# Performance work log

Hardware: AMD Instinct MI355X
Metric: run time of the kernel (lower is better)

Reference implementation:

```python
import jax, jax.numpy as jnp
import numpy as np

D = 64          # d_in
NH = [256, 256] # nn_depth_design
L = 16          # flow_layers
B = 32768       # batch of samples


def _build_masks():
    # Deterministic mask maps: this_min=0, this_max=d_in-1 for all layers
    mh0 = np.arange(NH[0]) % (D - 1)
    mh1 = np.arange(NH[1]) % (D - 1)
    M1 = (mh0[None, :] <= mh1[:, None]).astype(np.float32)  # [nh1, nh0]
    M0s, M2s = [], []
    for l in range(L):
        perm = np.arange(D) if l % 2 == 0 else np.arange(D)[::-1]
        M0s.append((perm[None, :] <= mh0[:, None]).astype(np.float32))  # [nh0, D]
        M2s.append((mh1[None, :] < perm[:, None]).astype(np.float32))  # [D, nh1]
    M0 = np.stack(M0s)                                   # [L, nh0, D]
    M1 = np.broadcast_to(M1, (L,) + M1.shape).copy()     # [L, nh1, nh0]
    M2 = np.stack(M2s)                                   # [L, D, nh1]
    return jnp.asarray(M0), jnp.asarray(M1), jnp.asarray(M2)


def setup_inputs() -> dict:
    key = jax.random.key(0)
    ks = jax.random.split(key, 13)
    u = jax.random.normal(ks[0], (B, D), dtype=jnp.float32)

    def w(k, shape, fan_in):
        return jax.random.uniform(k, shape, jnp.float32, -1.0, 1.0) / np.sqrt(fan_in)

    inp = {"u": u}
    i = 1
    for net in ("loc", "scale"):
        inp[f"{net}_W0"] = w(ks[i], (L, NH[0], D), D); i += 1
        inp[f"{net}_b0"] = w(ks[i], (L, NH[0]), D); i += 1
        inp[f"{net}_W1"] = w(ks[i], (L, NH[1], NH[0]), NH[0]); i += 1
        inp[f"{net}_b1"] = w(ks[i], (L, NH[1]), NH[0]); i += 1
        inp[f"{net}_W2"] = w(ks[i], (L, D, NH[1]), NH[1]); i += 1
        inp[f"{net}_b2"] = w(ks[i], (L, D), NH[1]); i += 1
    M0, M1, M2 = _build_masks()
    inp["M0"], inp["M1"], inp["M2"] = M0, M1, M2
    return inp


def reference(u, loc_W0, loc_b0, loc_W1, loc_b1, loc_W2, loc_b2,
              scale_W0, scale_b0, scale_W1, scale_b1, scale_W2, scale_b2,
              M0, M1, M2):
    def step(y, p):
        (lW0, lb0, lW1, lb1, lW2, lb2,
         sW0, sb0, sW1, sb1, sW2, sb2, m0, m1, m2) = p

        def net(W0, b0, W1, b1, W2, b2):
            h = jax.nn.relu(y @ (m0 * W0).T + b0)    # [B, nh0]
            h = jax.nn.relu(h @ (m1 * W1).T + b1)    # [B, nh1]
            return h @ (m2 * W2).T + b2              # [B, D]

        loc = net(lW0, lb0, lW1, lb1, lW2, lb2)
        sc = net(sW0, sb0, sW1, sb1, sW2, sb2)
        # inverse=False coupling: exp(-scale) * (y - loc)
        return jnp.exp(-sc) * (y - loc), None

    params = (loc_W0, loc_b0, loc_W1, loc_b1, loc_W2, loc_b2,
              scale_W0, scale_b0, scale_W1, scale_b1, scale_W2, scale_b2,
              M0, M1, M2)
    y, _ = jax.lax.scan(step, u, params)
    return y
```

## Files before the change

### kernel.cpp

```cpp
#include <hip/hip_runtime.h>
#include <hip/hip_bf16.h>

typedef __bf16 bf16x8 __attribute__((ext_vector_type(8)));
typedef __bf16 bf16x4 __attribute__((ext_vector_type(4)));
typedef float  f32x4  __attribute__((ext_vector_type(4)));

#define LAYERS 16
#define DIM 64
#define NHID 256
#define BATCH 32768
#define MTILE 64
#define NBLOCKS (BATCH / MTILE)

#define W0P_PER 16384
#define W1P_PER 65536
#define W2P_PER 16384
#define W0P_TOT (32 * W0P_PER)
#define W1P_TOT (32 * W1P_PER)
#define W2P_TOT (32 * W2P_PER)
#define PACK_TOT (W0P_TOT + W1P_TOT + W2P_TOT)

__global__ __launch_bounds__(256) void pack_weights(
    const float* __restrict__ lW0, const float* __restrict__ lW1, const float* __restrict__ lW2,
    const float* __restrict__ sW0, const float* __restrict__ sW1, const float* __restrict__ sW2,
    const float* __restrict__ M0,  const float* __restrict__ M1,  const float* __restrict__ M2,
    __bf16* __restrict__ ws)
{
    const long i = ((long)blockIdx.x * 256 + threadIdx.x) * 8;
    const float* W; const float* M; long src;
    if (i < W0P_TOT) {
        int netl = (int)(i / W0P_PER), rem = (int)(i % W0P_PER);
        int net = netl >> 4, l = netl & 15;
        int nt = rem >> 10, kt = (rem >> 9) & 1, lane = (rem >> 3) & 63;
        int n = nt * 16 + (lane & 15), k = kt * 32 + (lane >> 4) * 8;
        W = net ? sW0 : lW0; M = M0;
        src = (long)(l * 256 + n) * 64 + k;
    } else if (i < W0P_TOT + W1P_TOT) {
        long r = i - W0P_TOT;
        int netl = (int)(r / W1P_PER), rem = (int)(r % W1P_PER);
        int net = netl >> 4, l = netl & 15;
        int nt = rem >> 12, kt = (rem >> 9) & 7, lane = (rem >> 3) & 63;
        int n = nt * 16 + (lane & 15), k = kt * 32 + (lane >> 4) * 8;
        W = net ? sW1 : lW1; M = M1;
        src = (long)(l * 256 + n) * 256 + k;
    } else {
        long r = i - W0P_TOT - W1P_TOT;
        int netl = (int)(r / W2P_PER), rem = (int)(r % W2P_PER);
        int net = netl >> 4, l = netl & 15;
        int nt = rem >> 12, kt = (rem >> 9) & 7, lane = (rem >> 3) & 63;
        int n = nt * 16 + (lane & 15), k = kt * 32 + (lane >> 4) * 8;
        W = net ? sW2 : lW2; M = M2;
        src = (long)(l * 64 + n) * 256 + k;
    }
    f32x4 wa = *(const f32x4*)(W + src);
    f32x4 wb = *(const f32x4*)(W + src + 4);
    f32x4 ma = *(const f32x4*)(M + src);
    f32x4 mb = *(const f32x4*)(M + src + 4);
    bf16x8 o;
    o[0] = (__bf16)(wa[0] * ma[0]); o[1] = (__bf16)(wa[1] * ma[1]);
    o[2] = (__bf16)(wa[2] * ma[2]); o[3] = (__bf16)(wa[3] * ma[3]);
    o[4] = (__bf16)(wb[0] * mb[0]); o[5] = (__bf16)(wb[1] * mb[1]);
    o[6] = (__bf16)(wb[2] * mb[2]); o[7] = (__bf16)(wb[3] * mb[3]);
    *(bf16x8*)(ws + i) = o;
}

__global__ __launch_bounds__(512, 4) void flow_kernel(
    const float* __restrict__ u,
    const __bf16* __restrict__ wp,
    const float* __restrict__ lb0, const float* __restrict__ lb1, const float* __restrict__ lb2,
    const float* __restrict__ sb0, const float* __restrict__ sb1, const float* __restrict__ sb2,
    float* __restrict__ out)
{
    __shared__ __bf16 ybf[MTILE][72];
    __shared__ __bf16 buf1[MTILE][264];
    __shared__ __bf16 buf2[MTILE][264];

    const int tid  = threadIdx.x;
    const int wave = tid >> 6;
    const int lane = tid & 63;
    const int quad = lane >> 4;
    const int l16  = lane & 15;
    const int blk  = blockIdx.x;

    const int whid = wave * 2;
    const int mt3  = wave >> 1;
    const int ntb  = (wave & 1) * 2;

    const __bf16* w0p = wp;
    const __bf16* w1p = wp + W0P_TOT;
    const __bf16* w2p = wp + W0P_TOT + W1P_TOT;

    float y[2][4];
    #pragma unroll
    for (int ntl = 0; ntl < 2; ++ntl) {
        const float* src = u + (long)(blk * MTILE + (ntb + ntl) * 16 + l16) * DIM
                             + mt3 * 16 + quad * 4;
        f32x4 t = *(const f32x4*)src;
        #pragma unroll
        for (int r = 0; r < 4; ++r) y[ntl][r] = t[r];
    }

    for (int l = 0; l < LAYERS; ++l) {
        #pragma unroll
        for (int ntl = 0; ntl < 2; ++ntl) {
            bf16x4 v;
            #pragma unroll
            for (int r = 0; r < 4; ++r) v[r] = (__bf16)y[ntl][r];
            *(bf16x4*)&ybf[(ntb + ntl) * 16 + l16][mt3 * 16 + quad * 4] = v;
        }
        __syncthreads();

        float locr[2][4], scr[2][4];

        #pragma unroll
        for (int net = 0; net < 2; ++net) {
            const __bf16* w0b = w0p + (long)(net * 16 + l) * W0P_PER;
            const __bf16* w1b = w1p + (long)(net * 16 + l) * W1P_PER;
            const __bf16* w2b = w2p + (long)(net * 16 + l) * W2P_PER;
            const float* b0 = (net ? sb0 : lb0) + l * 256;
            const float* b1 = (net ? sb1 : lb1) + l * 256;
            const float* b2 = (net ? sb2 : lb2) + l * 64;

            {
                f32x4 acc[2][4];
                #pragma unroll
                for (int mt = 0; mt < 2; ++mt)
                    #pragma unroll
                    for (int nt = 0; nt < 4; ++nt)
                        acc[mt][nt] = (f32x4){0.f, 0.f, 0.f, 0.f};
                #pragma unroll
                for (int kt = 0; kt < 2; ++kt) {
                    bf16x8 aw[2], bv[4];
                    #pragma unroll
                    for (int mt = 0; mt < 2; ++mt)
                        aw[mt] = *(const bf16x8*)(w0b + (long)((whid + mt) * 2 + kt) * 512 + lane * 8);
                    #pragma unroll
                    for (int nt = 0; nt < 4; ++nt)
                        bv[nt] = *(const bf16x8*)&ybf[nt * 16 + l16][kt * 32 + quad * 8];
                    #pragma unroll
                    for (int mt = 0; mt < 2; ++mt)
                        #pragma unroll
                        for (int nt = 0; nt < 4; ++nt)
                            acc[mt][nt] = __builtin_amdgcn_mfma_f32_16x16x32_bf16(aw[mt], bv[nt], acc[mt][nt], 0, 0, 0);
                }
                #pragma unroll
                for (int mt = 0; mt < 2; ++mt) {
                    f32x4 bias = *(const f32x4*)(b0 + (whid + mt) * 16 + quad * 4);
                    #pragma unroll
                    for (int nt = 0; nt < 4; ++nt) {
                        bf16x4 v;
                        #pragma unroll
                        for (int r = 0; r < 4; ++r)
                            v[r] = (__bf16)fmaxf(acc[mt][nt][r] + bias[r], 0.f);
                        *(bf16x4*)&buf1[nt * 16 + l16][(whid + mt) * 16 + quad * 4] = v;
                    }
                }
            }
            __syncthreads();

            {
                f32x4 acc[2][4];
                #pragma unroll
                for (int mt = 0; mt < 2; ++mt)
                    #pragma unroll
                    for (int nt = 0; nt < 4; ++nt)
                        acc[mt][nt] = (f32x4){0.f, 0.f, 0.f, 0.f};
                #pragma unroll
                for (int kt = 0; kt < 8; ++kt) {
                    bf16x8 aw[2], bv[4];
                    #pragma unroll
                    for (int mt = 0; mt < 2; ++mt)
                        aw[mt] = *(const bf16x8*)(w1b + (long)((whid + mt) * 8 + kt) * 512 + lane * 8);
                    #pragma unroll
                    for (int nt = 0; nt < 4; ++nt)
                        bv[nt] = *(const bf16x8*)&buf1[nt * 16 + l16][kt * 32 + quad * 8];
                    #pragma unroll
                    for (int mt = 0; mt < 2; ++mt)
                        #pragma unroll
                        for (int nt = 0; nt < 4; ++nt)
                            acc[mt][nt] = __builtin_amdgcn_mfma_f32_16x16x32_bf16(aw[mt], bv[nt], acc[mt][nt], 0, 0, 0);
                }
                #pragma unroll
                for (int mt = 0; mt < 2; ++mt) {
                    f32x4 bias = *(const f32x4*)(b1 + (whid + mt) * 16 + quad * 4);
                    #pragma unroll
                    for (int nt = 0; nt < 4; ++nt) {
                        bf16x4 v;
                        #pragma unroll
                        for (int r = 0; r < 4; ++r)
                            v[r] = (__bf16)fmaxf(acc[mt][nt][r] + bias[r], 0.f);
                        *(bf16x4*)&buf2[nt * 16 + l16][(whid + mt) * 16 + quad * 4] = v;
                    }
                }
            }
            __syncthreads();

            {
                f32x4 acc[2];
                acc[0] = (f32x4){0.f, 0.f, 0.f, 0.f};
                acc[1] = (f32x4){0.f, 0.f, 0.f, 0.f};
                #pragma unroll
                for (int kt = 0; kt < 8; ++kt) {
                    bf16x8 aw = *(const bf16x8*)(w2b + (long)(mt3 * 8 + kt) * 512 + lane * 8);
                    #pragma unroll
                    for (int ntl = 0; ntl < 2; ++ntl) {
                        bf16x8 bv = *(const bf16x8*)&buf2[(ntb + ntl) * 16 + l16][kt * 32 + quad * 8];
                        acc[ntl] = __builtin_amdgcn_mfma_f32_16x16x32_bf16(aw, bv, acc[ntl], 0, 0, 0);
                    }
                }
                f32x4 bias = *(const f32x4*)(b2 + mt3 * 16 + quad * 4);
                if (net == 0) {
                    #pragma unroll
                    for (int ntl = 0; ntl < 2; ++ntl)
                        #pragma unroll
                        for (int r = 0; r < 4; ++r)
                            locr[ntl][r] = acc[ntl][r] + bias[r];
                } else {
                    #pragma unroll
                    for (int ntl = 0; ntl < 2; ++ntl)
                        #pragma unroll
                        for (int r = 0; r < 4; ++r)
                            scr[ntl][r] = acc[ntl][r] + bias[r];
                }
            }
        }

        #pragma unroll
        for (int ntl = 0; ntl < 2; ++ntl)
            #pragma unroll
            for (int r = 0; r < 4; ++r)
                y[ntl][r] = __expf(-scr[ntl][r]) * (y[ntl][r] - locr[ntl][r]);
    }

    #pragma unroll
    for (int ntl = 0; ntl < 2; ++ntl) {
        f32x4 t;
        #pragma unroll
        for (int r = 0; r < 4; ++r) t[r] = y[ntl][r];
        float* dst = out + (long)(blk * MTILE + (ntb + ntl) * 16 + l16) * DIM
                         + mt3 * 16 + quad * 4;
        *(f32x4*)dst = t;
    }
}

extern "C" void kernel_launch(void* const* d_in, const int* in_sizes, int n_in,
                              void* d_out, int out_size, void* d_ws, size_t ws_size,
                              hipStream_t stream) {
    const float* u   = (const float*)d_in[0];
    const float* lW0 = (const float*)d_in[1];
    const float* lb0 = (const float*)d_in[2];
    const float* lW1 = (const float*)d_in[3];
    const float* lb1 = (const float*)d_in[4];
    const float* lW2 = (const float*)d_in[5];
    const float* lb2 = (const float*)d_in[6];
    const float* sW0 = (const float*)d_in[7];
    const float* sb0 = (const float*)d_in[8];
    const float* sW1 = (const float*)d_in[9];
    const float* sb1 = (const float*)d_in[10];
    const float* sW2 = (const float*)d_in[11];
    const float* sb2 = (const float*)d_in[12];
    const float* M0  = (const float*)d_in[13];
    const float* M1  = (const float*)d_in[14];
    const float* M2  = (const float*)d_in[15];

    if (ws_size < (size_t)PACK_TOT * sizeof(__bf16)) return;
    __bf16* ws = (__bf16*)d_ws;

    pack_weights<<<PACK_TOT / 8 / 256, 256, 0, stream>>>(
        lW0, lW1, lW2, sW0, sW1, sW2, M0, M1, M2, ws);
    flow_kernel<<<NBLOCKS, 512, 0, stream>>>(
        u, ws, lb0, lb1, lb2, sb0, sb1, sb2, (float*)d_out);
}
```

Before: 369.7 us.

## Prefetch next-stage weight fragments into registers ahead of the barrier

Global weight fragments are now loaded one GEMM stage early. The first half of W1 is fetched during the W0 epilogue, W2 and the next W0 during the W1 epilogue, and the first W0 before the layer loop. This hides global and L2 load latency behind MFMA work and the __syncthreads barriers instead of stalling at the start of each GEMM. The cost is higher register pressure (about 20 extra bf16x8 values held), which could lower occupancy or cause spills. The next-W0 index wraps to layer 16 on the final iteration, which looks like an out-of-range read, though the result is never used.

```diff
diff --git a/kernel.cpp b/kernel.cpp
--- a/kernel.cpp
+++ b/kernel.cpp
@@ -19,6 +19,8 @@
 #define W1P_TOT (32 * W1P_PER)
 #define W2P_TOT (32 * W2P_PER)
 #define PACK_TOT (W0P_TOT + W1P_TOT + W2P_TOT)
+
+__device__ __forceinline__ bf16x8 ldw(const __bf16* p) { return *(const bf16x8*)p; }
 
 __global__ __launch_bounds__(256) void pack_weights(
     const float* __restrict__ lW0, const float* __restrict__ lW1, const float* __restrict__ lW2,
@@ -100,6 +102,13 @@
         for (int r = 0; r < 4; ++r) y[ntl][r] = t[r];
     }
 
+    bf16x8 wg1[4];
+    #pragma unroll
+    for (int mt = 0; mt < 2; ++mt)
+        #pragma unroll
+        for (int kt = 0; kt < 2; ++kt)
+            wg1[mt * 2 + kt] = ldw(w0p + (long)((whid + mt) * 2 + kt) * 512 + lane * 8);
+
     for (int l = 0; l < LAYERS; ++l) {
         #pragma unroll
         for (int ntl = 0; ntl < 2; ++ntl) {
@@ -114,13 +123,15 @@
 
         #pragma unroll
         for (int net = 0; net < 2; ++net) {
-            const __bf16* w0b = w0p + (long)(net * 16 + l) * W0P_PER;
             const __bf16* w1b = w1p + (long)(net * 16 + l) * W1P_PER;
             const __bf16* w2b = w2p + (long)(net * 16 + l) * W2P_PER;
+            const __bf16* w0n = w0p + (long)(net == 0 ? 16 + l : l + 1) * W0P_PER;
             const float* b0 = (net ? sb0 : lb0) + l * 256;
             const float* b1 = (net ? sb1 : lb1) + l * 256;
             const float* b2 = (net ? sb2 : lb2) + l * 64;
 
+            bf16x8 wg2a[8];
+
             {
                 f32x4 acc[2][4];
                 #pragma unroll
@@ -130,10 +141,7 @@
                         acc[mt][nt] = (f32x4){0.f, 0.f, 0.f, 0.f};
                 #pragma unroll
                 for (int kt = 0; kt < 2; ++kt) {
-                    bf16x8 aw[2], bv[4];
-                    #pragma unroll
-                    for (int mt = 0; mt < 2; ++mt)
-                        aw[mt] = *(const bf16x8*)(w0b + (long)((whid + mt) * 2 + kt) * 512 + lane * 8);
+                    bf16x8 bv[4];
                     #pragma unroll
                     for (int nt = 0; nt < 4; ++nt)
                         bv[nt] = *(const bf16x8*)&ybf[nt * 16 + l16][kt * 32 + quad * 8];
@@ -141,8 +149,13 @@
                     for (int mt = 0; mt < 2; ++mt)
                         #pragma unroll
                         for (int nt = 0; nt < 4; ++nt)
-                            acc[mt][nt] = __builtin_amdgcn_mfma_f32_16x16x32_bf16(aw[mt], bv[nt], acc[mt][nt], 0, 0, 0);
-                }
+                            acc[mt][nt] = __builtin_amdgcn_mfma_f32_16x16x32_bf16(wg1[mt * 2 + kt], bv[nt], acc[mt][nt], 0, 0, 0);
+                }
+                #pragma unroll
+                for (int kt = 0; kt < 4; ++kt)
+                    #pragma unroll
+                    for (int mt = 0; mt < 2; ++mt)
+                        wg2a[kt * 2 + mt] = ldw(w1b + (long)((whid + mt) * 8 + kt) * 512 + lane * 8);
                 #pragma unroll
                 for (int mt = 0; mt < 2; ++mt) {
                     f32x4 bias = *(const f32x4*)(b0 + (whid + mt) * 16 + quad * 4);
@@ -158,6 +171,8 @@
             }
             __syncthreads();
 
+            bf16x8 wg3[8];
+
             {
                 f32x4 acc[2][4];
                 #pragma unroll
@@ -167,10 +182,12 @@
                         acc[mt][nt] = (f32x4){0.f, 0.f, 0.f, 0.f};
                 #pragma unroll
                 for (int kt = 0; kt < 8; ++kt) {
-                    bf16x8 aw[2], bv[4];
-                    #pragma unroll
-                    for (int mt = 0; mt < 2; ++mt)
-                        aw[mt] = *(const bf16x8*)(w1b + (long)((whid + mt) * 8 + kt) * 512 + lane * 8);
+                    bf16x8 aw[2];
+                    #pragma unroll
+                    for (int mt = 0; mt < 2; ++mt)
+                        aw[mt] = (kt < 4) ? wg2a[kt * 2 + mt]
+                                          : ldw(w1b + (long)((whid + mt) * 8 + kt) * 512 + lane * 8);
+                    bf16x8 bv[4];
                     #pragma unroll
                     for (int nt = 0; nt < 4; ++nt)
                         bv[nt] = *(const bf16x8*)&buf1[nt * 16 + l16][kt * 32 + quad * 8];
@@ -180,6 +197,14 @@
                         for (int nt = 0; nt < 4; ++nt)
                             acc[mt][nt] = __builtin_amdgcn_mfma_f32_16x16x32_bf16(aw[mt], bv[nt], acc[mt][nt], 0, 0, 0);
                 }
+                #pragma unroll
+                for (int kt = 0; kt < 8; ++kt)
+                    wg3[kt] = ldw(w2b + (long)(mt3 * 8 + kt) * 512 + lane * 8);
+                #pragma unroll
+                for (int mt = 0; mt < 2; ++mt)
+                    #pragma unroll
+                    for (int kt = 0; kt < 2; ++kt)
+                        wg1[mt * 2 + kt] = ldw(w0n + (long)((whid + mt) * 2 + kt) * 512 + lane * 8);
                 #pragma unroll
                 for (int mt = 0; mt < 2; ++mt) {
                     f32x4 bias = *(const f32x4*)(b1 + (whid + mt) * 16 + quad * 4);
@@ -201,11 +226,10 @@
                 acc[1] = (f32x4){0.f, 0.f, 0.f, 0.f};
                 #pragma unroll
                 for (int kt = 0; kt < 8; ++kt) {
-                    bf16x8 aw = *(const bf16x8*)(w2b + (long)(mt3 * 8 + kt) * 512 + lane * 8);
                     #pragma unroll
                     for (int ntl = 0; ntl < 2; ++ntl) {
                         bf16x8 bv = *(const bf16x8*)&buf2[(ntb + ntl) * 16 + l16][kt * 32 + quad * 8];
-                        acc[ntl] = __builtin_amdgcn_mfma_f32_16x16x32_bf16(aw, bv, acc[ntl], 0, 0, 0);
+                        acc[ntl] = __builtin_amdgcn_mfma_f32_16x16x32_bf16(wg3[kt], bv, acc[ntl], 0, 0, 0);
                     }
                 }
                 f32x4 bias = *(const f32x4*)(b2 + mt3 * 16 + quad * 4);
```

Result: faster. 349.9 us (-5.4%).

## Double waves per block and halve per-wave MFMA tile

Applied to the files above, without the earlier changes.

Launches 1024-thread blocks so 16 waves split each 64-row tile: each wave computes a 2x2 grid of 16x16 tiles in the hidden layers and one 16x16 tile in the output layer. This raises parallelism and latency hiding per block and reduces per-wave register pressure. In exchange, each weight fragment is now loaded by two waves (one per batch half), so global/L2 weight traffic and barrier cost grow.

```diff
diff --git a/kernel.cpp b/kernel.cpp
--- a/kernel.cpp
+++ b/kernel.cpp
@@ -19,6 +19,8 @@
 #define W1P_TOT (32 * W1P_PER)
 #define W2P_TOT (32 * W2P_PER)
 #define PACK_TOT (W0P_TOT + W1P_TOT + W2P_TOT)
+
+__device__ __forceinline__ bf16x8 ldw(const __bf16* p) { return *(const bf16x8*)p; }
 
 __global__ __launch_bounds__(256) void pack_weights(
     const float* __restrict__ lW0, const float* __restrict__ lW1, const float* __restrict__ lW2,
@@ -64,7 +66,7 @@
     *(bf16x8*)(ws + i) = o;
 }
 
-__global__ __launch_bounds__(512, 4) void flow_kernel(
+__global__ __launch_bounds__(1024, 8) void flow_kernel(
     const float* __restrict__ u,
     const __bf16* __restrict__ wp,
     const float* __restrict__ lb0, const float* __restrict__ lb1, const float* __restrict__ lb2,
@@ -82,35 +84,28 @@
     const int l16  = lane & 15;
     const int blk  = blockIdx.x;
 
-    const int whid = wave * 2;
-    const int mt3  = wave >> 1;
-    const int ntb  = (wave & 1) * 2;
+    const int g   = wave >> 1;
+    const int p   = wave & 1;
+    const int ot3 = wave >> 2;
+    const int bt3 = wave & 3;
 
     const __bf16* w0p = wp;
     const __bf16* w1p = wp + W0P_TOT;
     const __bf16* w2p = wp + W0P_TOT + W1P_TOT;
 
-    float y[2][4];
-    #pragma unroll
-    for (int ntl = 0; ntl < 2; ++ntl) {
-        const float* src = u + (long)(blk * MTILE + (ntb + ntl) * 16 + l16) * DIM
-                             + mt3 * 16 + quad * 4;
-        f32x4 t = *(const f32x4*)src;
-        #pragma unroll
-        for (int r = 0; r < 4; ++r) y[ntl][r] = t[r];
-    }
+    f32x4 y = *(const f32x4*)(u + (long)(blk * MTILE + bt3 * 16 + l16) * DIM
+                                + ot3 * 16 + quad * 4);
 
     for (int l = 0; l < LAYERS; ++l) {
-        #pragma unroll
-        for (int ntl = 0; ntl < 2; ++ntl) {
+        {
             bf16x4 v;
             #pragma unroll
-            for (int r = 0; r < 4; ++r) v[r] = (__bf16)y[ntl][r];
-            *(bf16x4*)&ybf[(ntb + ntl) * 16 + l16][mt3 * 16 + quad * 4] = v;
+            for (int r = 0; r < 4; ++r) v[r] = (__bf16)y[r];
+            *(bf16x4*)&ybf[bt3 * 16 + l16][ot3 * 16 + quad * 4] = v;
         }
         __syncthreads();
 
-        float locr[2][4], scr[2][4];
+        f32x4 locr, scr;
 
         #pragma unroll
         for (int net = 0; net < 2; ++net) {
@@ -122,125 +117,105 @@
             const float* b2 = (net ? sb2 : lb2) + l * 64;
 
             {
-                f32x4 acc[2][4];
-                #pragma unroll
-                for (int mt = 0; mt < 2; ++mt)
-                    #pragma unroll
-                    for (int nt = 0; nt < 4; ++nt)
-                        acc[mt][nt] = (f32x4){0.f, 0.f, 0.f, 0.f};
+                f32x4 acc[2][2];
+                #pragma unroll
+                for (int o = 0; o < 2; ++o)
+                    #pragma unroll
+                    for (int b = 0; b < 2; ++b)
+                        acc[o][b] = (f32x4){0.f, 0.f, 0.f, 0.f};
                 #pragma unroll
                 for (int kt = 0; kt < 2; ++kt) {
-                    bf16x8 aw[2], bv[4];
-                    #pragma unroll
-                    for (int mt = 0; mt < 2; ++mt)
-                        aw[mt] = *(const bf16x8*)(w0b + (long)((whid + mt) * 2 + kt) * 512 + lane * 8);
-                    #pragma unroll
-                    for (int nt = 0; nt < 4; ++nt)
-                        bv[nt] = *(const bf16x8*)&ybf[nt * 16 + l16][kt * 32 + quad * 8];
-                    #pragma unroll
-                    for (int mt = 0; mt < 2; ++mt)
-                        #pragma unroll
-                        for (int nt = 0; nt < 4; ++nt)
-                            acc[mt][nt] = __builtin_amdgcn_mfma_f32_16x16x32_bf16(aw[mt], bv[nt], acc[mt][nt], 0, 0, 0);
-                }
-                #pragma unroll
-                for (int mt = 0; mt < 2; ++mt) {
-                    f32x4 bias = *(const f32x4*)(b0 + (whid + mt) * 16 + quad * 4);
-                    #pragma unroll
-                    for (int nt = 0; nt < 4; ++nt) {
+                    bf16x8 aw[2], bv[2];
+                    #pragma unroll
+                    for (int o = 0; o < 2; ++o)
+                        aw[o] = ldw(w0b + (long)((2 * g + o) * 2 + kt) * 512 + lane * 8);
+                    #pragma unroll
+                    for (int b = 0; b < 2; ++b)
+                        bv[b] = *(const bf16x8*)&ybf[(2 * p + b) * 16 + l16][kt * 32 + quad * 8];
+                    #pragma unroll
+                    for (int o = 0; o < 2; ++o)
+                        #pragma unroll
+                        for (int b = 0; b < 2; ++b)
+                            acc[o][b] = __builtin_amdgcn_mfma_f32_16x16x32_bf16(aw[o], bv[b], acc[o][b], 0, 0, 0);
+                }
+                #pragma unroll
+                for (int o = 0; o < 2; ++o) {
+                    f32x4 bias = *(const f32x4*)(b0 + (2 * g + o) * 16 + quad * 4);
+                    #pragma unroll
+                    for (int b = 0; b < 2; ++b) {
                         bf16x4 v;
                         #pragma unroll
                         for (int r = 0; r < 4; ++r)
-                            v[r] = (__bf16)fmaxf(acc[mt][nt][r] + bias[r], 0.f);
-                        *(bf16x4*)&buf1[nt * 16 + l16][(whid + mt) * 16 + quad * 4] = v;
+                            v[r] = (__bf16)fmaxf(acc[o][b][r] + bias[r], 0.f);
+                        *(bf16x4*)&buf1[(2 * p + b) * 16 + l16][(2 * g + o) * 16 + quad * 4] = v;
                     }
                 }
             }
             __syncthreads();
 
             {
-                f32x4 acc[2][4];
-                #pragma unroll
-                for (int mt = 0; mt < 2; ++mt)
-                    #pragma unroll
-                    for (int nt = 0; nt < 4; ++nt)
-                        acc[mt][nt] = (f32x4){0.f, 0.f, 0.f, 0.f};
+                f32x4 acc[2][2];
+                #pragma unroll
+                for (int o = 0; o < 2; ++o)
+                    #pragma unroll
+                    for (int b = 0; b < 2; ++b)
+                        acc[o][b] = (f32x4){0.f, 0.f, 0.f, 0.f};
                 #pragma unroll
                 for (int kt = 0; kt < 8; ++kt) {
-                    bf16x8 aw[2], bv[4];
-                    #pragma unroll
-                    for (int mt = 0; mt < 2; ++mt)
-                        aw[mt] = *(const bf16x8*)(w1b + (long)((whid + mt) * 8 + kt) * 512 + lane * 8);
-                    #pragma unroll
-                    for (int nt = 0; nt < 4; ++nt)
-                        bv[nt] = *(const bf16x8*)&buf1[nt * 16 + l16][kt * 32 + quad * 8];
-                    #pragma unroll
-                    for (int mt = 0; mt < 2; ++mt)
-                        #pragma unroll
-                        for (int nt = 0; nt < 4; ++nt)
-                            acc[mt][nt] = __builtin_amdgcn_mfma_f32_16x16x32_bf16(aw[mt], bv[nt], acc[mt][nt], 0, 0, 0);
-                }
-                #pragma unroll
-                for (int mt = 0; mt < 2; ++mt) {
-                    f32x4 bias = *(const f32x4*)(b1 + (whid + mt) * 16 + quad * 4);
-                    #pragma unroll
-                    for (int nt = 0; nt < 4; ++nt) {
+                    bf16x8 aw[2], bv[2];
+                    #pragma unroll
+                    for (int o = 0; o < 2; ++o)
+                        aw[o] = ldw(w1b + (long)((2 * g + o) * 8 + kt) * 512 + lane * 8);
+                    #pragma unroll
+                    for (int b = 0; b < 2; ++b)
+                        bv[b] = *(const bf16x8*)&buf1[(2 * p + b) * 16 + l16][kt * 32 + quad * 8];
+                    #pragma unroll
+                    for (int o = 0; o < 2; ++o)
+                        #pragma unroll
+                        for (int b = 0; b < 2; ++b)
+                            acc[o][b] = __builtin_amdgcn_mfma_f32_16x16x32_bf16(aw[o], bv[b], acc[o][b], 0, 0, 0);
+                }
+                #pragma unroll
+                for (int o = 0; o < 2; ++o) {
+                    f32x4 bias = *(const f32x4*)(b1 + (2 * g + o) * 16 + quad * 4);
+                    #pragma unroll
+                    for (int b = 0; b < 2; ++b) {
                         bf16x4 v;
                         #pragma unroll
                         for (int r = 0; r < 4; ++r)
-                            v[r] = (__bf16)fmaxf(acc[mt][nt][r] + bias[r], 0.f);
-                        *(bf16x4*)&buf2[nt * 16 + l16][(whid + mt) * 16 + quad * 4] = v;
+                            v[r] = (__bf16)fmaxf(acc[o][b][r] + bias[r], 0.f);
+                        *(bf16x4*)&buf2[(2 * p + b) * 16 + l16][(2 * g + o) * 16 + quad * 4] = v;
                     }
                 }
             }
             __syncthreads();
 
             {
-                f32x4 acc[2];
-                acc[0] = (f32x4){0.f, 0.f, 0.f, 0.f};
-                acc[1] = (f32x4){0.f, 0.f, 0.f, 0.f};
+                f32x4 acc = (f32x4){0.f, 0.f, 0.f, 0.f};
                 #pragma unroll
                 for (int kt = 0; kt < 8; ++kt) {
-                    bf16x8 aw = *(const bf16x8*)(w2b + (long)(mt3 * 8 + kt) * 512 + lane * 8);
-                    #pragma unroll
-                    for (int ntl = 0; ntl < 2; ++ntl) {
-                        bf16x8 bv = *(const bf16x8*)&buf2[(ntb + ntl) * 16 + l16][kt * 32 + quad * 8];
-                        acc[ntl] = __builtin_amdgcn_mfma_f32_16x16x32_bf16(aw, bv, acc[ntl], 0, 0, 0);
-                    }
-                }
-                f32x4 bias = *(const f32x4*)(b2 + mt3 * 16 + quad * 4);
+                    bf16x8 aw = ldw(w2b + (long)(ot3 * 8 + kt) * 512 + lane * 8);
+                    bf16x8 bv = *(const bf16x8*)&buf2[bt3 * 16 + l16][kt * 32 + quad * 8];
+                    acc = __builtin_amdgcn_mfma_f32_16x16x32_bf16(aw, bv, acc, 0, 0, 0);
+                }
+                f32x4 bias = *(const f32x4*)(b2 + ot3 * 16 + quad * 4);
                 if (net == 0) {
                     #pragma unroll
-                    for (int ntl = 0; ntl < 2; ++ntl)
-                        #pragma unroll
-                        for (int r = 0; r < 4; ++r)
-                            locr[ntl][r] = acc[ntl][r] + bias[r];
+                    for (int r = 0; r < 4; ++r) locr[r] = acc[r] + bias[r];
                 } else {
                     #pragma unroll
-                    for (int ntl = 0; ntl < 2; ++ntl)
-                        #pragma unroll
-                        for (int r = 0; r < 4; ++r)
-                            scr[ntl][r] = acc[ntl][r] + bias[r];
+                    for (int r = 0; r < 4; ++r) scr[r] = acc[r] + bias[r];
                 }
             }
         }
 
         #pragma unroll
-        for (int ntl = 0; ntl < 2; ++ntl)
-            #pragma unroll
-            for (int r = 0; r < 4; ++r)
-                y[ntl][r] = __expf(-scr[ntl][r]) * (y[ntl][r] - locr[ntl][r]);
+        for (int r = 0; r < 4; ++r)
+            y[r] = __expf(-scr[r]) * (y[r] - locr[r]);
     }
 
-    #pragma unroll
-    for (int ntl = 0; ntl < 2; ++ntl) {
-        f32x4 t;
-        #pragma unroll
-        for (int r = 0; r < 4; ++r) t[r] = y[ntl][r];
-        float* dst = out + (long)(blk * MTILE + (ntb + ntl) * 16 + l16) * DIM
-                         + mt3 * 16 + quad * 4;
-        *(f32x4*)dst = t;
-    }
+    *(f32x4*)(out + (long)(blk * MTILE + bt3 * 16 + l16) * DIM
+                  + ot3 * 16 + quad * 4) = y;
 }
 
 extern "C" void kernel_launch(void* const* d_in, const int* in_sizes, int n_in,
@@ -268,6 +243,6 @@
 
     pack_weights<<<PACK_TOT / 8 / 256, 256, 0, stream>>>(
         lW0, lW1, lW2, sW0, sW1, sW2, M0, M1, M2, ws);
-    flow_kernel<<<NBLOCKS, 512, 0, stream>>>(
+    flow_kernel<<<NBLOCKS, 1024, 0, stream>>>(
         u, ws, lb0, lb1, lb2, sb0, sb1, sb2, (float*)d_out);
 }
```

Result: slower. 574.7 us (+55.5%).
